# Optimization experiments

Hardware: AMD Instinct MI355X
Metric: run time of the kernel (lower is better)

Reference implementation:

```python
import jax, jax.numpy as jnp
import numpy as np

EPS = 1e-6
NH, HD, D, FF = 4, 128, 512, 2048
SCALE = HD ** -0.5


def rms(x, w):
    return x * jax.lax.rsqrt(jnp.mean(x * x, axis=-1, keepdims=True) + EPS) * w


def adaln(x, emb, w, b, nw):
    e = jax.nn.silu(emb) @ w.T + b  # [B, 6D]
    sm, cm, gm, sp, cp, gp = jnp.split(e, 6, axis=-1)
    y = rms(x, nw) * (1.0 + cm[:, None]) + sm[:, None]
    return y, gm, sp, cp, gp


def apply_rope(x, rope):
    # x: [B,H,N,HD], rope: [N,1,HD] (even slots cos-source, odd slots sin-source)
    f = rope[:, 0]  # [N, HD]
    cos = jnp.repeat(f[:, 0::2], 2, axis=-1)[None, None]  # [1,1,N,HD]
    sin = jnp.repeat(f[:, 1::2], 2, axis=-1)[None, None]
    xr = x.reshape(*x.shape[:-1], -1, 2)
    rot = jnp.stack([-xr[..., 1], xr[..., 0]], axis=-1).reshape(x.shape)
    return x * cos + rot * sin


def sdpa(q, k, v, scale):
    s = jnp.einsum('bhqd,bhkd->bhqk', q, k) * scale
    p = jax.nn.softmax(s, axis=-1)
    return jnp.einsum('bhqk,bhkd->bhqd', p, v)


def mlp(x, w1, b1, w2, b2):
    h = jax.nn.gelu(x @ w1.T + b1, approximate=True)
    return h @ w2.T + b2


def setup_inputs() -> dict:
    key = jax.random.key(0)
    ks = jax.random.split(key, 32)
    B, L, Hh, Ww = 2, 512, 64, 32
    N = Hh * Ww
    s = 1.0 / np.sqrt(D)
    sf = 1.0 / np.sqrt(FF)
    rn = lambda k, sh, sc=1.0: jax.random.normal(k, sh, jnp.float32) * sc
    # RoPE buffer: per-pair angles, even slots cos, odd slots sin
    pos = jnp.arange(N, dtype=jnp.float32)
    inv = 1.0 / (10000.0 ** (jnp.arange(0, HD, 2, dtype=jnp.float32) / HD))
    ang = pos[:, None] * inv[None, :]  # [N, HD//2]
    rope = jnp.zeros((N, 1, HD), jnp.float32)
    rope = rope.at[:, 0, 0::2].set(jnp.cos(ang)).at[:, 0, 1::2].set(jnp.sin(ang))
    return {
        'txt': rn(ks[0], (B, L, D)),
        'img': rn(ks[1], (B, N, D)),
        'vec': rn(ks[2], (B, D)),
        'rope': rope,
        'sol_temperature': jax.random.uniform(ks[3], (B, NH), jnp.float32) + 0.5,
        'sol_spatial': rn(ks[4], (B, 8, 8)),
        'img_adaln_w': rn(ks[5], (6 * D, D), s), 'img_adaln_b': rn(ks[6], (6 * D,), 0.02),
        'img_adaln_norm_w': jnp.ones((D,), jnp.float32),
        'txt_adaln_w': rn(ks[7], (6 * D, D), s), 'txt_adaln_b': rn(ks[8], (6 * D,), 0.02),
        'txt_adaln_norm_w': jnp.ones((D,), jnp.float32),
        'txt_qkv_w': rn(ks[9], (3 * NH * HD, D), s),
        'img_qkv_w': rn(ks[10], (3 * NH * HD, D), s),
        'txt_out_w': rn(ks[11], (D, NH * HD), s),
        'img_out_w': rn(ks[12], (D, NH * HD), s),
        'sol_mod_w': rn(ks[13], (NH,), 0.1), 'sol_mod_b': rn(ks[14], (NH,), 0.1),
        'img_norm2_w': jnp.ones((D,), jnp.float32),
        'txt_norm2_w': jnp.ones((D,), jnp.float32),
        'img_fc1_w': rn(ks[15], (FF, D), s), 'img_fc1_b': rn(ks[16], (FF,), 0.02),
        'img_fc2_w': rn(ks[17], (D, FF), sf), 'img_fc2_b': rn(ks[18], (D,), 0.02),
        'txt_fc1_w': rn(ks[19], (FF, D), s), 'txt_fc1_b': rn(ks[20], (FF,), 0.02),
        'txt_fc2_w': rn(ks[21], (D, FF), sf), 'txt_fc2_b': rn(ks[22], (D,), 0.02),
        'H': Hh, 'W': Ww,
    }


def reference(txt, img, vec, rope, sol_temperature, sol_spatial,
              img_adaln_w, img_adaln_b, img_adaln_norm_w,
              txt_adaln_w, txt_adaln_b, txt_adaln_norm_w,
              txt_qkv_w, img_qkv_w, txt_out_w, img_out_w,
              sol_mod_w, sol_mod_b, img_norm2_w, txt_norm2_w,
              img_fc1_w, img_fc1_b, img_fc2_w, img_fc2_b,
              txt_fc1_w, txt_fc1_b, txt_fc2_w, txt_fc2_b, H, W):
    B, L, _ = txt.shape
    N = img.shape[1]
    img_n, img_g, img_sh, img_sc, img_gm = adaln(img, vec, img_adaln_w, img_adaln_b, img_adaln_norm_w)
    txt_n, txt_g, txt_sh, txt_sc, txt_gm = adaln(txt, vec, txt_adaln_w, txt_adaln_b, txt_adaln_norm_w)
    # joint attention
    tqkv = (txt_n @ txt_qkv_w.T).reshape(B, L, 3, NH, HD)
    iqkv = (img_n @ img_qkv_w.T).reshape(B, N, 3, NH, HD)
    tq, tk, tv = [jnp.transpose(tqkv[:, :, i], (0, 2, 1, 3)) for i in range(3)]
    iq, ik, iv = [jnp.transpose(iqkv[:, :, i], (0, 2, 1, 3)) for i in range(3)]
    iq = apply_rope(iq, rope)
    ik = apply_rope(ik, rope)
    # spatial prior modulation (1x1 conv over bilinear-upsampled prior)
    sol_up = jax.image.resize(sol_spatial[:, None], (B, 1, H, W), method='bilinear')
    mod = sol_up * sol_mod_w[None, :, None, None] + sol_mod_b[None, :, None, None]  # [B,NH,H,W]
    mod = jnp.exp(jnp.clip(mod.reshape(B, NH, H * W), -2.0, 2.0))
    iq = iq * mod[..., None]
    ik = ik * mod[..., None]
    k = jnp.concatenate([tk, ik], axis=2)  # [B,NH,L+N,HD]
    v = jnp.concatenate([tv, iv], axis=2)
    txt_att = sdpa(tq, k, v, SCALE)
    txt_att = jnp.transpose(txt_att, (0, 2, 1, 3)).reshape(B, L, NH * HD) @ txt_out_w.T
    # temperature-rescaled image attention
    temp = jnp.maximum(jnp.mean(sol_temperature, axis=1, keepdims=True), 0.1)  # [B,1]
    eff = (SCALE / temp)[:, :, None, None]  # [B,1,1,1]
    img_att = sdpa(iq * jnp.sqrt(eff), k * jnp.sqrt(eff), v, 1.0)
    img_att = jnp.transpose(img_att, (0, 2, 1, 3)).reshape(B, N, NH * HD) @ img_out_w.T
    txt = txt + txt_g[:, None] * txt_att
    img = img + img_g[:, None] * img_att
    txt_in = rms(txt, txt_norm2_w) * (1.0 + txt_sc[:, None]) + txt_sh[:, None]
    img_in = rms(img, img_norm2_w) * (1.0 + img_sc[:, None]) + img_sh[:, None]
    txt = txt + txt_gm[:, None] * mlp(txt_in, txt_fc1_w, txt_fc1_b, txt_fc2_w, txt_fc2_b)
    img = img + img_gm[:, None] * mlp(img_in, img_fc1_w, img_fc1_b, img_fc2_w, img_fc2_b)
    return (txt, img)
```

## Files before the change

### kernel.cpp

```cpp
#include <hip/hip_runtime.h>
#include <math.h>

typedef unsigned short ushort_t;

constexpr int B_  = 2;
constexpr int L_  = 512;
constexpr int N_  = 2048;
constexpr int T_  = 2560;
constexpr int D_  = 512;
constexpr int NH_ = 4;
constexpr int HD_ = 128;
constexpr int FF_ = 2048;
constexpr int SIXD = 3072;
constexpr int MROWS = B_ * T_;
#define SCALE_ 0.08838834764831843f

constexpr size_t QSZ    = (size_t)B_ * NH_ * T_ * HD_;
constexpr size_t O_ETXT = 0;
constexpr size_t O_EIMG = O_ETXT + (size_t)B_ * SIXD;
constexpr size_t O_MOD  = O_EIMG + (size_t)B_ * SIXD;
constexpr size_t O_EFF  = O_MOD + (size_t)B_ * NH_ * N_;
constexpr size_t O_XN   = O_EFF + 16;
constexpr size_t O_Q    = O_XN + QSZ;
constexpr size_t O_K    = O_Q + QSZ;
constexpr size_t O_V    = O_K + QSZ;
constexpr size_t O_ATTN = O_V + QSZ;
constexpr size_t O_X2   = O_ATTN + QSZ;
constexpr size_t O_XIN2 = O_X2 + QSZ;
constexpr size_t O_H    = O_Q;
constexpr size_t O_ML   = O_X2 + QSZ / 2;

constexpr size_t WQ_STREAM = (size_t)SIXD / 2 * D_;
constexpr size_t WQ_TOTAL  = 2 * WQ_STREAM;
constexpr size_t WM_PROJ   = 0;
constexpr size_t WM_PROJ_S = (size_t)D_ * D_;
constexpr size_t WM_FC1    = WM_PROJ + 2 * WM_PROJ_S;
constexpr size_t WM_FC1_S  = (size_t)FF_ * D_;
constexpr size_t WM_FC2    = WM_FC1 + 2 * WM_FC1_S;
constexpr size_t WM_FC2_S  = (size_t)D_ * FF_;

typedef short bf16x8 __attribute__((ext_vector_type(8)));
typedef float f32x4 __attribute__((ext_vector_type(4)));

__device__ __forceinline__ ushort_t f2bf_rne(float x) {
  unsigned u = __float_as_uint(x);
  u += 0x7fff + ((u >> 16) & 1);
  return (ushort_t)(u >> 16);
}

__device__ __forceinline__ void gload_lds16(const ushort_t* g, ushort_t* l) {
  __builtin_amdgcn_global_load_lds(
      (const __attribute__((address_space(1))) void*)g,
      (__attribute__((address_space(3))) void*)l, 16, 0, 0);
}

__global__ __launch_bounds__(256) void k_stage0(
    const float* __restrict__ vec,
    const float* __restrict__ wt, const float* __restrict__ bt,
    const float* __restrict__ wi, const float* __restrict__ bi,
    const float* __restrict__ sspat, const float* __restrict__ mw,
    const float* __restrict__ mb, const float* __restrict__ stemp,
    const float* __restrict__ qkvwt, const float* __restrict__ qkvwi,
    float* __restrict__ ws) {
  int blk = blockIdx.x;
  if (blk < 48) {
    int s = blk / 24;
    int rem = blk % 24;
    int b = rem / 12;
    int o = (rem % 12) * 256 + threadIdx.x;
    __shared__ float sv[D_];
    for (int i = threadIdx.x; i < D_; i += 256) {
      float x = vec[b * D_ + i];
      sv[i] = x / (1.0f + __expf(-x));
    }
    __syncthreads();
    const float* w = (s == 0) ? wt : wi;
    const float* bb = (s == 0) ? bt : bi;
    const float4* wrow = (const float4*)(w + (size_t)o * D_);
    float acc = 0.f;
    for (int d4 = 0; d4 < D_ / 4; ++d4) {
      float4 wv = wrow[d4];
      int d = d4 * 4;
      acc += wv.x * sv[d] + wv.y * sv[d + 1] + wv.z * sv[d + 2] + wv.w * sv[d + 3];
    }
    acc += bb[o];
    float* e = ws + ((s == 0) ? O_ETXT : O_EIMG);
    e[b * SIXD + o] = acc;
  } else if (blk < 112) {
    int idx = (blk - 48) * 256 + threadIdx.x;
    if (idx < B_) {
      float s = 0.f;
      for (int h = 0; h < NH_; ++h) s += stemp[idx * NH_ + h];
      float t = fmaxf(s * 0.25f, 0.1f);
      ws[O_EFF + idx] = SCALE_ / t;
    }
    int b = idx / (NH_ * N_);
    int h = (idx / N_) % NH_;
    int n = idx % N_;
    int y = n >> 5;
    int x = n & 31;
    float fy = (y + 0.5f) * 0.125f - 0.5f;
    float fx = (x + 0.5f) * 0.25f  - 0.5f;
    float y0f = floorf(fy), x0f = floorf(fx);
    float wy = fy - y0f, wx = fx - x0f;
    int y0 = (int)y0f, x0 = (int)x0f;
    int iy0 = y0 < 0 ? 0 : y0, iy1 = (y0 + 1) > 7 ? 7 : (y0 + 1);
    int ix0 = x0 < 0 ? 0 : x0, ix1 = (x0 + 1) > 7 ? 7 : (x0 + 1);
    const float* S = sspat + b * 64;
    float v00 = S[iy0*8+ix0], v01 = S[iy0*8+ix1];
    float v10 = S[iy1*8+ix0], v11 = S[iy1*8+ix1];
    float up = (1.f-wy)*((1.f-wx)*v00 + wx*v01) + wy*((1.f-wx)*v10 + wx*v11);
    float m = up * mw[h] + mb[h];
    m = fminf(fmaxf(m, -2.f), 2.f);
    ws[O_MOD + idx] = __expf(m);
  } else {
    int g = (blk - 112) * 256 + threadIdx.x;
    int s = g >= (int)(WQ_STREAM / 4);
    const float4* src = (const float4*)(s ? qkvwi : qkvwt);
    float4 v = src[g - s * (int)(WQ_STREAM / 4)];
    ushort4 hh, ll;
    hh.x = f2bf_rne(v.x); hh.y = f2bf_rne(v.y); hh.z = f2bf_rne(v.z); hh.w = f2bf_rne(v.w);
    ll.x = f2bf_rne(v.x - __uint_as_float((unsigned)hh.x << 16));
    ll.y = f2bf_rne(v.y - __uint_as_float((unsigned)hh.y << 16));
    ll.z = f2bf_rne(v.z - __uint_as_float((unsigned)hh.z << 16));
    ll.w = f2bf_rne(v.w - __uint_as_float((unsigned)hh.w << 16));
    ushort_t* Wqh = (ushort_t*)(ws + O_ATTN);
    ushort_t* Wql = Wqh + WQ_TOTAL;
    *(ushort4*)&Wqh[(size_t)g * 4] = hh;
    *(ushort4*)&Wql[(size_t)g * 4] = ll;
  }
}

template<bool FROM_INPUT>
__global__ __launch_bounds__(256) void k_rmsmod(const float* __restrict__ txt, const float* __restrict__ img,
                                                const float* __restrict__ src_ws,
                                                const float* __restrict__ nw_txt, const float* __restrict__ nw_img,
                                                int sh_off, int sc_off,
                                                const float* __restrict__ e_ws,
                                                ushort_t* __restrict__ oh, ushort_t* __restrict__ ol) {
  int row = blockIdx.x;
  int b = row / T_;
  int t = row % T_;
  bool is_txt = t < L_;
  int i0 = threadIdx.x * 2;
  float x0, x1;
  if (FROM_INPUT) {
    const float* src = is_txt ? (txt + ((size_t)b * L_ + t) * D_)
                              : (img + ((size_t)b * N_ + (t - L_)) * D_);
    x0 = src[i0]; x1 = src[i0 + 1];
  } else {
    const float* src = src_ws + (size_t)row * D_;
    x0 = src[i0]; x1 = src[i0 + 1];
  }
  float ss = x0 * x0 + x1 * x1;
  for (int off = 32; off; off >>= 1) ss += __shfl_down(ss, off, 64);
  __shared__ float red[4];
  if ((threadIdx.x & 63) == 0) red[threadIdx.x >> 6] = ss;
  __syncthreads();
  float tot = red[0] + red[1] + red[2] + red[3];
  float r = rsqrtf(tot * (1.0f / D_) + 1e-6f);
  const float* e = e_ws + (is_txt ? O_ETXT : O_EIMG) + (size_t)b * SIXD;
  const float* nw = is_txt ? nw_txt : nw_img;
  float y0 = x0 * r * nw[i0]     * (1.f + e[sc_off + i0])     + e[sh_off + i0];
  float y1 = x1 * r * nw[i0 + 1] * (1.f + e[sc_off + i0 + 1]) + e[sh_off + i0 + 1];
  ushort_t h0 = f2bf_rne(y0), h1 = f2bf_rne(y1);
  ushort_t l0 = f2bf_rne(y0 - __uint_as_float((unsigned)h0 << 16));
  ushort_t l1 = f2bf_rne(y1 - __uint_as_float((unsigned)h1 << 16));
  *(unsigned*)&oh[(size_t)row * D_ + i0] = (unsigned)h0 | ((unsigned)h1 << 16);
  *(unsigned*)&ol[(size_t)row * D_ + i0] = (unsigned)l0 | ((unsigned)l1 << 16);
}

template<int NTILE, int NTERMS, int KDIM, int NPR, int EPI>
__global__ __launch_bounds__(256) void k_gemm(
    const ushort_t* __restrict__ Aph, const ushort_t* __restrict__ Apl,
    const ushort_t* __restrict__ Wth, const ushort_t* __restrict__ Wtl,
    const ushort_t* __restrict__ Wih, const ushort_t* __restrict__ Wil,
    const float* __restrict__ biast, const float* __restrict__ biasi,
    const float* __restrict__ ws_ro, float* __restrict__ wsw,
    const float* __restrict__ txt, const float* __restrict__ img,
    ushort_t* __restrict__ Hph, ushort_t* __restrict__ Hpl, float* __restrict__ outf) {
  int mt = blockIdx.x / NPR, nt = blockIdx.x % NPR;
  int row0 = mt * 128;
  int col0 = nt * NTILE;
  int b = row0 / T_;
  int t0 = row0 % T_;
  bool is_txt = t0 < L_;
  const ushort_t* Wh = is_txt ? Wth : Wih;
  const ushort_t* Wl = (NTERMS == 3) ? (is_txt ? Wtl : Wil) : nullptr;

  __shared__ __align__(16) ushort_t ash[128 * 32];
  __shared__ __align__(16) ushort_t asl[128 * 32];
  __shared__ __align__(16) ushort_t bsh[NTILE * 32];
  __shared__ __align__(16) ushort_t bsl[(NTERMS == 3) ? NTILE * 32 : 8];

  int tid = threadIdx.x;
  int w = tid >> 6, lane = tid & 63, quad = lane >> 4, lc = lane & 15;
  int rh = w >> 1, ch = w & 1;
  constexpr int NFR = NTILE / 32;

  int Rloc  = lane >> 2;
  int lslot = (lane & 3) ^ ((lane >> 3) & 3);
  int ssw = (quad ^ ((lc >> 1) & 3)) * 8;

  f32x4 acc[4][NFR];
  #pragma unroll
  for (int m = 0; m < 4; ++m)
    #pragma unroll
    for (int n = 0; n < NFR; ++n) acc[m][n] = f32x4{0.f, 0.f, 0.f, 0.f};

  for (int kt = 0; kt < KDIM / 32; ++kt) {
    int scol = kt * 32 + lslot * 8;
    #pragma unroll
    for (int cc = 0; cc < 2; ++cc) {
      int c = w * 2 + cc;
      size_t goff = (size_t)(row0 + c * 16 + Rloc) * KDIM + scol;
      gload_lds16(Aph + goff, &ash[c * 512]);
      gload_lds16(Apl + goff, &asl[c * 512]);
    }
    #pragma unroll
    for (int cc = 0; cc < NTILE / 64; ++cc) {
      int c = w + cc * 4;
      size_t goff = (size_t)(col0 + c * 16 + Rloc) * KDIM + scol;
      gload_lds16(Wh + goff, &bsh[c * 512]);
      if (NTERMS == 3) gload_lds16(Wl + goff, &bsl[c * 512]);
    }
    __syncthreads();

    bf16x8 afh[4], afl[4];
    #pragma unroll
    for (int m = 0; m < 4; ++m) {
      int ar = rh * 64 + m * 16 + lc;
      afh[m] = *(const bf16x8*)&ash[ar * 32 + ssw];
      afl[m] = *(const bf16x8*)&asl[ar * 32 + ssw];
    }
    #pragma unroll
    for (int n = 0; n < NFR; ++n) {
      int br = ch * (NTILE / 2) + n * 16 + lc;
      bf16x8 bh = *(const bf16x8*)&bsh[br * 32 + ssw];
      if (NTERMS == 3) {
        bf16x8 bl = *(const bf16x8*)&bsl[br * 32 + ssw];
        #pragma unroll
        for (int m = 0; m < 4; ++m) {
          acc[m][n] = __builtin_amdgcn_mfma_f32_16x16x32_bf16(afl[m], bh, acc[m][n], 0, 0, 0);
          acc[m][n] = __builtin_amdgcn_mfma_f32_16x16x32_bf16(afh[m], bl, acc[m][n], 0, 0, 0);
          acc[m][n] = __builtin_amdgcn_mfma_f32_16x16x32_bf16(afh[m], bh, acc[m][n], 0, 0, 0);
        }
      } else {
        #pragma unroll
        for (int m = 0; m < 4; ++m) {
          acc[m][n] = __builtin_amdgcn_mfma_f32_16x16x32_bf16(afl[m], bh, acc[m][n], 0, 0, 0);
          acc[m][n] = __builtin_amdgcn_mfma_f32_16x16x32_bf16(afh[m], bh, acc[m][n], 0, 0, 0);
        }
      }
    }
    __syncthreads();
  }

  const float* e = ws_ro + (is_txt ? O_ETXT : O_EIMG) + (size_t)b * SIXD;
  const float* bias = is_txt ? biast : biasi;
  #pragma unroll
  for (int m = 0; m < 4; ++m) {
    #pragma unroll
    for (int n = 0; n < NFR; ++n) {
      #pragma unroll
      for (int r = 0; r < 4; ++r) {
        int rg = row0 + rh * 64 + m * 16 + quad * 4 + r;
        int cg = col0 + ch * (NTILE / 2) + n * 16 + lc;
        float val = acc[m][n][r];
        int tt = rg % T_;
        if (EPI == 0) {
          int which = cg >> 9, h = (cg >> 7) & 3, dd = cg & 127;
          float* dst = wsw + (which == 0 ? O_Q : which == 1 ? O_K : O_V)
                     + (((size_t)b * NH_ + h) * T_ + tt) * HD_ + dd;
          *dst = val;
        } else if (EPI == 1) {
          float g = e[1024 + cg];
          float res = is_txt ? txt[((size_t)b * L_ + tt) * D_ + cg]
                             : img[((size_t)b * N_ + (tt - L_)) * D_ + cg];
          wsw[O_X2 + (size_t)rg * D_ + cg] = res + g * val;
        } else if (EPI == 2) {
          float x = val + bias[cg];
          float z = 0.7978845608028654f * (x + 0.044715f * x * x * x);
          z = fminf(fmaxf(z, -40.f), 40.f);
          float u = __expf(-2.f * z);
          float th = (1.f - u) / (1.f + u);
          float hv = 0.5f * x * (1.f + th);
          ushort_t hh = f2bf_rne(hv);
          Hph[(size_t)rg * FF_ + cg] = hh;
          Hpl[(size_t)rg * FF_ + cg] = f2bf_rne(hv - __uint_as_float((unsigned)hh << 16));
        } else {
          float g = e[2560 + cg];
          float v2 = ws_ro[O_X2 + (size_t)rg * D_ + cg] + g * (val + bias[cg]);
          size_t oi = is_txt ? ((size_t)b * L_ + tt) * D_ + cg
                             : (size_t)B_ * L_ * D_ + ((size_t)b * N_ + (tt - L_)) * D_ + cg;
          outf[oi] = v2;
        }
      }
    }
  }
}

__global__ __launch_bounds__(256) void k_stage1(
    float* __restrict__ ws, const float* __restrict__ rope,
    const float* __restrict__ pw_t, const float* __restrict__ pw_i,
    const float* __restrict__ f1_t, const float* __restrict__ f1_i,
    const float* __restrict__ f2_t, const float* __restrict__ f2_i) {
  int blk = blockIdx.x;
  if (blk < 5120) {
    int idx = blk * 256 + threadIdx.x;
    int i = idx & 63;
    int p = idx >> 6;
    int t = p % T_;
    int bh = p / T_;
    size_t base = (size_t)p * HD_ + 2 * i;
    float* Q = ws + O_Q;
    float* K = ws + O_K;
    float k0 = K[base], k1 = K[base + 1];
    if (t >= L_) {
      int n = t - L_;
      float c = rope[(size_t)n * HD_ + 2 * i];
      float s = rope[(size_t)n * HD_ + 2 * i + 1];
      float m = ws[O_MOD + (size_t)bh * N_ + n];
      float q0 = Q[base], q1 = Q[base + 1];
      Q[base]     = (q0 * c - q1 * s) * m;
      Q[base + 1] = (q1 * c + q0 * s) * m;
      float nk0 = (k0 * c - k1 * s) * m;
      float nk1 = (k1 * c + k0 * s) * m;
      k0 = nk0; k1 = nk1;
    }
    ushort_t h0 = f2bf_rne(k0), h1 = f2bf_rne(k1);
    ushort_t l0 = f2bf_rne(k0 - __uint_as_float((unsigned)h0 << 16));
    ushort_t l1 = f2bf_rne(k1 - __uint_as_float((unsigned)h1 << 16));
    ushort_t* KH = (ushort_t*)(ws + O_XIN2);
    ushort_t* KL = KH + QSZ;
    *(unsigned*)&KH[(size_t)p * HD_ + 2 * i] = (unsigned)h0 | ((unsigned)h1 << 16);
    *(unsigned*)&KL[(size_t)p * HD_ + 2 * i] = (unsigned)l0 | ((unsigned)l1 << 16);
  } else if (blk < 5440) {
    int vblk = blk - 5120;
    int bh = vblk & 7;
    int tt = vblk >> 3;
    int t0 = tt * 64;
    __shared__ ushort_t vls[128 * 72];
    int tid = threadIdx.x;
    {
      int tr = tid & 63, dc = tid >> 6;
      const float4* src = (const float4*)(ws + O_V + ((size_t)bh * T_ + t0 + tr) * HD_ + dc * 32);
      #pragma unroll
      for (int f = 0; f < 8; ++f) {
        float4 v = src[f];
        int d = dc * 32 + f * 4;
        vls[(d + 0) * 72 + tr] = f2bf_rne(v.x);
        vls[(d + 1) * 72 + tr] = f2bf_rne(v.y);
        vls[(d + 2) * 72 + tr] = f2bf_rne(v.z);
        vls[(d + 3) * 72 + tr] = f2bf_rne(v.w);
      }
    }
    __syncthreads();
    {
      int d = tid >> 1, th = (tid & 1) * 32;
      unsigned* Vt32 = (unsigned*)(ws + O_X2);
      size_t obase = (((size_t)bh * HD_ + d) * T_ + t0 + th) >> 1;
      #pragma unroll
      for (int k = 0; k < 16; ++k) {
        unsigned lo = vls[d * 72 + th + 2 * k];
        unsigned hi = vls[d * 72 + th + 2 * k + 1];
        Vt32[obase + k] = lo | (hi << 16);
      }
    }
  } else {
    int g = (blk - 5440) * 256 + threadIdx.x;
    const float* src; int local;
    if (g < 65536)        { src = pw_t; local = g; }
    else if (g < 131072)  { src = pw_i; local = g - 65536; }
    else if (g < 393216)  { src = f1_t; local = g - 131072; }
    else if (g < 655360)  { src = f1_i; local = g - 393216; }
    else if (g < 917504)  { src = f2_t; local = g - 655360; }
    else                  { src = f2_i; local = g - 917504; }
    float4 v = ((const float4*)src)[local];
    ushort4 hh;
    hh.x = f2bf_rne(v.x); hh.y = f2bf_rne(v.y); hh.z = f2bf_rne(v.z); hh.w = f2bf_rne(v.w);
    ushort_t* Wm = (ushort_t*)(ws + O_XN);
    *(ushort4*)&Wm[(size_t)g * 4] = hh;
  }
}

__global__ __launch_bounds__(256) void k_attn7(const float* __restrict__ ws_ro, float* __restrict__ wsw) {
  int bh = blockIdx.x & 7;
  int rest = blockIdx.x >> 3;
  int qg = rest % 40;
  int ks = rest / 40;
  int kt0 = (ks == 0) ? 0 : (ks == 1) ? 14 : 27;
  int kt1 = (ks == 0) ? 14 : (ks == 1) ? 27 : 40;
  int b = bh >> 2;
  int tid = threadIdx.x;
  int w = tid >> 6, lane = tid & 63, quad = lane >> 4, lc = lane & 15;
  int q0 = (qg * 4 + w) * 16;
  float scale = (q0 < L_) ? SCALE_ : ws_ro[O_EFF + b];

  const ushort_t* Khs = (const ushort_t*)(ws_ro + O_XIN2);
  const ushort_t* Kls = Khs + QSZ;
  const ushort_t* Vts = (const ushort_t*)(ws_ro + O_X2) + (size_t)bh * HD_ * T_;

  __shared__ __align__(16) ushort_t ksh[64 * 136];
  __shared__ __align__(16) ushort_t ksl[64 * 136];
  __shared__ __align__(16) ushort_t ps[4 * 16 * 72];
  ushort_t* pw = &ps[w * 1152];

  bf16x8 qh[4], ql[4];
  {
    const float* qrowp = ws_ro + O_Q + ((size_t)bh * T_ + q0 + lc) * HD_ + quad * 8;
    #pragma unroll
    for (int k2 = 0; k2 < 4; ++k2) {
      float4 a = *(const float4*)(qrowp + k2 * 32);
      float4 c = *(const float4*)(qrowp + k2 * 32 + 4);
      float v[8] = {a.x, a.y, a.z, a.w, c.x, c.y, c.z, c.w};
      #pragma unroll
      for (int e = 0; e < 8; ++e) {
        float x = v[e] * scale;
        ushort_t hh = f2bf_rne(x);
        float hf = __uint_as_float((unsigned)hh << 16);
        qh[k2][e] = (short)hh;
        ql[k2][e] = (short)f2bf_rne(x - hf);
      }
    }
  }

  f32x4 o[8];
  #pragma unroll
  for (int i = 0; i < 8; ++i) o[i] = f32x4{0.f, 0.f, 0.f, 0.f};
  float m_r[4] = {-1e30f, -1e30f, -1e30f, -1e30f};
  float l_r[4] = {0.f, 0.f, 0.f, 0.f};

  for (int kt = kt0; kt < kt1; ++kt) {
    {
      int row = tid >> 2, cs = tid & 3;
      size_t gbase = ((size_t)bh * T_ + kt * 64 + row) * HD_;
      #pragma unroll
      for (int cc = 0; cc < 4; ++cc) {
        int c = cs + cc * 4;
        *(uint4*)&ksh[row * 136 + c * 8] = *(const uint4*)&Khs[gbase + c * 8];
        *(uint4*)&ksl[row * 136 + c * 8] = *(const uint4*)&Kls[gbase + c * 8];
      }
    }
    __syncthreads();

    f32x4 s[4];
    #pragma unroll
    for (int nt = 0; nt < 4; ++nt) s[nt] = f32x4{0.f, 0.f, 0.f, 0.f};
    #pragma unroll
    for (int k2 = 0; k2 < 4; ++k2) {
      int ko = k2 * 32 + quad * 8;
      #pragma unroll
      for (int nt = 0; nt < 4; ++nt) {
        bf16x8 kh = *(const bf16x8*)&ksh[(nt * 16 + lc) * 136 + ko];
        bf16x8 kl = *(const bf16x8*)&ksl[(nt * 16 + lc) * 136 + ko];
        s[nt] = __builtin_amdgcn_mfma_f32_16x16x32_bf16(ql[k2], kh, s[nt], 0, 0, 0);
        s[nt] = __builtin_amdgcn_mfma_f32_16x16x32_bf16(qh[k2], kl, s[nt], 0, 0, 0);
        s[nt] = __builtin_amdgcn_mfma_f32_16x16x32_bf16(qh[k2], kh, s[nt], 0, 0, 0);
      }
    }

    const ushort_t* Vb = Vts + kt * 64;
    bf16x8 vb0[8];
    #pragma unroll
    for (int dt = 0; dt < 8; ++dt)
      vb0[dt] = *(const bf16x8*)&Vb[(size_t)(dt * 16 + lc) * T_ + quad * 8];

    float alpha[4];
    #pragma unroll
    for (int r = 0; r < 4; ++r) {
      float rm = fmaxf(fmaxf(s[0][r], s[1][r]), fmaxf(s[2][r], s[3][r]));
      rm = fmaxf(rm, __shfl_xor(rm, 1, 64));
      rm = fmaxf(rm, __shfl_xor(rm, 2, 64));
      rm = fmaxf(rm, __shfl_xor(rm, 4, 64));
      rm = fmaxf(rm, __shfl_xor(rm, 8, 64));
      float mn = fmaxf(m_r[r], rm);
      alpha[r] = __expf(m_r[r] - mn);
      m_r[r] = mn;
      float p0 = __expf(s[0][r] - mn);
      float p1 = __expf(s[1][r] - mn);
      float p2 = __expf(s[2][r] - mn);
      float p3 = __expf(s[3][r] - mn);
      float rs = (p0 + p1) + (p2 + p3);
      rs += __shfl_xor(rs, 1, 64);
      rs += __shfl_xor(rs, 2, 64);
      rs += __shfl_xor(rs, 4, 64);
      rs += __shfl_xor(rs, 8, 64);
      l_r[r] = l_r[r] * alpha[r] + rs;
      int prow = quad * 4 + r;
      pw[prow * 72 + lc]      = f2bf_rne(p0);
      pw[prow * 72 + lc + 16] = f2bf_rne(p1);
      pw[prow * 72 + lc + 32] = f2bf_rne(p2);
      pw[prow * 72 + lc + 48] = f2bf_rne(p3);
    }
    #pragma unroll
    for (int dt = 0; dt < 8; ++dt) {
      #pragma unroll
      for (int r = 0; r < 4; ++r) o[dt][r] *= alpha[r];
    }

    bf16x8 vb1[8];
    #pragma unroll
    for (int dt = 0; dt < 8; ++dt)
      vb1[dt] = *(const bf16x8*)&Vb[(size_t)(dt * 16 + lc) * T_ + 32 + quad * 8];

    bf16x8 pa0 = *(const bf16x8*)&pw[lc * 72 + quad * 8];
    bf16x8 pa1 = *(const bf16x8*)&pw[lc * 72 + 32 + quad * 8];
    #pragma unroll
    for (int dt = 0; dt < 8; ++dt)
      o[dt] = __builtin_amdgcn_mfma_f32_16x16x32_bf16(pa0, vb0[dt], o[dt], 0, 0, 0);
    #pragma unroll
    for (int dt = 0; dt < 8; ++dt)
      o[dt] = __builtin_amdgcn_mfma_f32_16x16x32_bf16(pa1, vb1[dt], o[dt], 0, 0, 0);
    __syncthreads();
  }

  float* OP = wsw + ((ks == 0) ? O_K : (ks == 1) ? O_V : O_ATTN);
  float* ML = wsw + O_ML;
  int trow0 = q0 + quad * 4;
  #pragma unroll
  for (int r = 0; r < 4; ++r) {
    size_t base = ((size_t)bh * T_ + (trow0 + r)) * HD_ + lc;
    #pragma unroll
    for (int dt = 0; dt < 8; ++dt) OP[base + dt * 16] = o[dt][r];
    if (lc == 0) {
      size_t mi = (((size_t)ks * 8 + bh) * T_ + (trow0 + r)) * 2;
      ML[mi]     = m_r[r];
      ML[mi + 1] = l_r[r];
    }
  }
}

__global__ __launch_bounds__(256) void k_comb(const float* __restrict__ ws_ro, float* __restrict__ wsw) {
  int bh = blockIdx.x & 7;
  int qg = blockIdx.x >> 3;
  int b = bh >> 2, h = bh & 3;
  int q0 = qg * 64;
  int tid = threadIdx.x;
  __shared__ float wls[64][4];
  if (tid < 64) {
    const float* ML = ws_ro + O_ML;
    size_t r0 = ((size_t)0 * 8 + bh) * T_ + q0 + tid;
    size_t r1 = ((size_t)1 * 8 + bh) * T_ + q0 + tid;
    size_t r2 = ((size_t)2 * 8 + bh) * T_ + q0 + tid;
    float m0 = ML[r0 * 2], l0 = ML[r0 * 2 + 1];
    float m1 = ML[r1 * 2], l1 = ML[r1 * 2 + 1];
    float m2 = ML[r2 * 2], l2 = ML[r2 * 2 + 1];
    float mm = fmaxf(fmaxf(m0, m1), m2);
    float w0 = __expf(m0 - mm), w1 = __expf(m1 - mm), w2 = __expf(m2 - mm);
    float inv = 1.0f / (w0 * l0 + w1 * l1 + w2 * l2);
    wls[tid][0] = w0 * inv; wls[tid][1] = w1 * inv; wls[tid][2] = w2 * inv; wls[tid][3] = 0.f;
  }
  __syncthreads();
  const float* P0 = ws_ro + O_K;
  const float* P1 = ws_ro + O_V;
  const float* P2 = ws_ro + O_ATTN;
  ushort_t* ATh = (ushort_t*)(wsw + O_Q);
  ushort_t* ATl = ATh + QSZ;
  #pragma unroll
  for (int it = 0; it < 8; ++it) {
    int idx = it * 256 + tid;
    int row = idx >> 5;
    int d4 = (idx & 31) * 4;
    size_t pb = ((size_t)bh * T_ + q0 + row) * HD_ + d4;
    float4 a = *(const float4*)&P0[pb];
    float4 c = *(const float4*)&P1[pb];
    float4 d = *(const float4*)&P2[pb];
    float w0 = wls[row][0], w1 = wls[row][1], w2 = wls[row][2];
    float v[4] = {a.x * w0 + c.x * w1 + d.x * w2,
                  a.y * w0 + c.y * w1 + d.y * w2,
                  a.z * w0 + c.z * w1 + d.z * w2,
                  a.w * w0 + c.w * w1 + d.w * w2};
    ushort4 hh, ll;
    ushort_t* hp = (ushort_t*)&hh; ushort_t* lp = (ushort_t*)&ll;
    #pragma unroll
    for (int j = 0; j < 4; ++j) {
      ushort_t hv = f2bf_rne(v[j]);
      hp[j] = hv;
      lp[j] = f2bf_rne(v[j] - __uint_as_float((unsigned)hv << 16));
    }
    size_t ob = ((size_t)b * T_ + q0 + row) * D_ + h * HD_ + d4;
    *(ushort4*)&ATh[ob] = hh;
    *(ushort4*)&ATl[ob] = ll;
  }
}

extern "C" void kernel_launch(void* const* d_in, const int* in_sizes, int n_in,
                              void* d_out, int out_size, void* d_ws, size_t ws_size,
                              hipStream_t stream) {
  (void)in_sizes; (void)n_in; (void)out_size; (void)ws_size;
  const float* txt    = (const float*)d_in[0];
  const float* img    = (const float*)d_in[1];
  const float* vec    = (const float*)d_in[2];
  const float* rope   = (const float*)d_in[3];
  const float* stemp  = (const float*)d_in[4];
  const float* sspat  = (const float*)d_in[5];
  const float* i_aw   = (const float*)d_in[6];
  const float* i_ab   = (const float*)d_in[7];
  const float* i_anw  = (const float*)d_in[8];
  const float* t_aw   = (const float*)d_in[9];
  const float* t_ab   = (const float*)d_in[10];
  const float* t_anw  = (const float*)d_in[11];
  const float* t_qkvw = (const float*)d_in[12];
  const float* i_qkvw = (const float*)d_in[13];
  const float* t_outw = (const float*)d_in[14];
  const float* i_outw = (const float*)d_in[15];
  const float* modw   = (const float*)d_in[16];
  const float* modb   = (const float*)d_in[17];
  const float* i_n2w  = (const float*)d_in[18];
  const float* t_n2w  = (const float*)d_in[19];
  const float* i_f1w  = (const float*)d_in[20];
  const float* i_f1b  = (const float*)d_in[21];
  const float* i_f2w  = (const float*)d_in[22];
  const float* i_f2b  = (const float*)d_in[23];
  const float* t_f1w  = (const float*)d_in[24];
  const float* t_f1b  = (const float*)d_in[25];
  const float* t_f2w  = (const float*)d_in[26];
  const float* t_f2b  = (const float*)d_in[27];
  float* ws = (float*)d_ws;
  float* out = (float*)d_out;
  ushort_t* XNh  = (ushort_t*)(ws + O_XN);   ushort_t* XNl  = XNh + QSZ;
  ushort_t* XI2h = (ushort_t*)(ws + O_XIN2); ushort_t* XI2l = XI2h + QSZ;
  ushort_t* Hh   = (ushort_t*)(ws + O_H);    ushort_t* Hl   = Hh + 4 * QSZ;
  ushort_t* ATh  = (ushort_t*)(ws + O_Q);    ushort_t* ATl  = ATh + QSZ;
  ushort_t* Wqh = (ushort_t*)(ws + O_ATTN);  ushort_t* Wql = Wqh + WQ_TOTAL;
  ushort_t* Wm  = (ushort_t*)(ws + O_XN);

  hipLaunchKernelGGL(k_stage0, dim3(48 + 64 + 1536), dim3(256), 0, stream,
                     vec, t_aw, t_ab, i_aw, i_ab, sspat, modw, modb, stemp,
                     t_qkvw, i_qkvw, ws);
  hipLaunchKernelGGL((k_rmsmod<true>), dim3(MROWS), dim3(256), 0, stream,
                     txt, img, (const float*)nullptr, t_anw, i_anw, 0, 512, ws, XNh, XNl);
  hipLaunchKernelGGL((k_gemm<128, 3, 512, 12, 0>), dim3(40 * 12), dim3(256), 0, stream,
                     XNh, XNl, Wqh, Wql, Wqh + WQ_STREAM, Wql + WQ_STREAM,
                     nullptr, nullptr, ws, ws, txt, img,
                     (ushort_t*)nullptr, (ushort_t*)nullptr, nullptr);
  hipLaunchKernelGGL(k_stage1, dim3(5120 + 320 + 4608), dim3(256), 0, stream,
                     ws, rope, t_outw, i_outw, t_f1w, i_f1w, t_f2w, i_f2w);
  hipLaunchKernelGGL(k_attn7, dim3(960), dim3(256), 0, stream, ws, ws);
  hipLaunchKernelGGL(k_comb, dim3(320), dim3(256), 0, stream, ws, ws);
  hipLaunchKernelGGL((k_gemm<64, 2, 512, 8, 1>), dim3(40 * 8), dim3(256), 0, stream,
                     ATh, ATl, Wm + WM_PROJ, nullptr, Wm + WM_PROJ + WM_PROJ_S, nullptr,
                     nullptr, nullptr, ws, ws, txt, img,
                     (ushort_t*)nullptr, (ushort_t*)nullptr, nullptr);
  hipLaunchKernelGGL((k_rmsmod<false>), dim3(MROWS), dim3(256), 0, stream,
                     (const float*)nullptr, (const float*)nullptr, ws + O_X2, t_n2w, i_n2w,
                     1536, 2048, ws, XI2h, XI2l);
  hipLaunchKernelGGL((k_gemm<128, 2, 512, 16, 2>), dim3(40 * 16), dim3(256), 0, stream,
                     XI2h, XI2l, Wm + WM_FC1, nullptr, Wm + WM_FC1 + WM_FC1_S, nullptr,
                     t_f1b, i_f1b, ws, ws, txt, img, Hh, Hl, nullptr);
  hipLaunchKernelGGL((k_gemm<64, 2, 2048, 8, 3>), dim3(40 * 8), dim3(256), 0, stream,
                     Hh, Hl, Wm + WM_FC2, nullptr, Wm + WM_FC2 + WM_FC2_S, nullptr,
                     t_f2b, i_f2b, ws, ws, txt, img,
                     (ushort_t*)nullptr, (ushort_t*)nullptr, out);
}
```

Before: 490.3 us.

## Prefetch next K tile into LDS via direct global-to-LDS loads with XOR swizzle

The attention kernel now loads K hi/lo tiles straight from global memory into LDS using direct-to-LDS 16-byte loads. The padded row stride is replaced by an XOR-swizzled unpadded layout to avoid bank conflicts. The load for the next key tile is issued right after the QK^T MFMAs, so it overlaps with the softmax and PV work of the current tile and hides global latency. This relies on correct wait/barrier placement before the next iteration reads the buffer.

```diff
diff --git a/kernel.cpp b/kernel.cpp
--- a/kernel.cpp
+++ b/kernel.cpp
@@ -384,7 +384,7 @@
   }
 }
 
-__global__ __launch_bounds__(256) void k_attn7(const float* __restrict__ ws_ro, float* __restrict__ wsw) {
+__global__ __launch_bounds__(256) void k_attn10(const float* __restrict__ ws_ro, float* __restrict__ wsw) {
   int bh = blockIdx.x & 7;
   int rest = blockIdx.x >> 3;
   int qg = rest % 40;
@@ -401,10 +401,13 @@
   const ushort_t* Kls = Khs + QSZ;
   const ushort_t* Vts = (const ushort_t*)(ws_ro + O_X2) + (size_t)bh * HD_ * T_;
 
-  __shared__ __align__(16) ushort_t ksh[64 * 136];
-  __shared__ __align__(16) ushort_t ksl[64 * 136];
+  __shared__ __align__(16) ushort_t ksh[64 * 128];
+  __shared__ __align__(16) ushort_t ksl[64 * 128];
   __shared__ __align__(16) ushort_t ps[4 * 16 * 72];
   ushort_t* pw = &ps[w * 1152];
+
+  int rloc = lane >> 4;
+  int sst  = lane & 15;
 
   bf16x8 qh[4], ql[4];
   {
@@ -431,32 +434,47 @@
   float m_r[4] = {-1e30f, -1e30f, -1e30f, -1e30f};
   float l_r[4] = {0.f, 0.f, 0.f, 0.f};
 
+  {
+    size_t gRow = (size_t)bh * T_ + kt0 * 64;
+    #pragma unroll
+    for (int j = 0; j < 4; ++j) {
+      int r0 = w * 16 + j * 4;
+      int lslot = sst ^ (j * 4 + rloc);
+      size_t goff = (gRow + r0 + rloc) * HD_ + (size_t)lslot * 8;
+      gload_lds16(Khs + goff, &ksh[r0 * 128]);
+      gload_lds16(Kls + goff, &ksl[r0 * 128]);
+    }
+  }
+  __syncthreads();
+
   for (int kt = kt0; kt < kt1; ++kt) {
-    {
-      int row = tid >> 2, cs = tid & 3;
-      size_t gbase = ((size_t)bh * T_ + kt * 64 + row) * HD_;
-      #pragma unroll
-      for (int cc = 0; cc < 4; ++cc) {
-        int c = cs + cc * 4;
-        *(uint4*)&ksh[row * 136 + c * 8] = *(const uint4*)&Khs[gbase + c * 8];
-        *(uint4*)&ksl[row * 136 + c * 8] = *(const uint4*)&Kls[gbase + c * 8];
-      }
-    }
-    __syncthreads();
-
     f32x4 s[4];
     #pragma unroll
     for (int nt = 0; nt < 4; ++nt) s[nt] = f32x4{0.f, 0.f, 0.f, 0.f};
     #pragma unroll
     for (int k2 = 0; k2 < 4; ++k2) {
-      int ko = k2 * 32 + quad * 8;
       #pragma unroll
       for (int nt = 0; nt < 4; ++nt) {
-        bf16x8 kh = *(const bf16x8*)&ksh[(nt * 16 + lc) * 136 + ko];
-        bf16x8 kl = *(const bf16x8*)&ksl[(nt * 16 + lc) * 136 + ko];
+        int row = nt * 16 + lc;
+        int so = ((k2 * 4 + quad) ^ lc) * 8;
+        bf16x8 kh = *(const bf16x8*)&ksh[row * 128 + so];
+        bf16x8 kl = *(const bf16x8*)&ksl[row * 128 + so];
         s[nt] = __builtin_amdgcn_mfma_f32_16x16x32_bf16(ql[k2], kh, s[nt], 0, 0, 0);
         s[nt] = __builtin_amdgcn_mfma_f32_16x16x32_bf16(qh[k2], kl, s[nt], 0, 0, 0);
         s[nt] = __builtin_amdgcn_mfma_f32_16x16x32_bf16(qh[k2], kh, s[nt], 0, 0, 0);
+      }
+    }
+    __syncthreads();
+
+    if (kt + 1 < kt1) {
+      size_t gRow = (size_t)bh * T_ + (kt + 1) * 64;
+      #pragma unroll
+      for (int j = 0; j < 4; ++j) {
+        int r0 = w * 16 + j * 4;
+        int lslot = sst ^ (j * 4 + rloc);
+        size_t goff = (gRow + r0 + rloc) * HD_ + (size_t)lslot * 8;
+        gload_lds16(Khs + goff, &ksh[r0 * 128]);
+        gload_lds16(Kls + goff, &ksl[r0 * 128]);
       }
     }
 
@@ -637,7 +655,7 @@
                      (ushort_t*)nullptr, (ushort_t*)nullptr, nullptr);
   hipLaunchKernelGGL(k_stage1, dim3(5120 + 320 + 4608), dim3(256), 0, stream,
                      ws, rope, t_outw, i_outw, t_f1w, i_f1w, t_f2w, i_f2w);
-  hipLaunchKernelGGL(k_attn7, dim3(960), dim3(256), 0, stream, ws, ws);
+  hipLaunchKernelGGL(k_attn10, dim3(960), dim3(256), 0, stream, ws, ws);
   hipLaunchKernelGGL(k_comb, dim3(320), dim3(256), 0, stream, ws, ws);
   hipLaunchKernelGGL((k_gemm<64, 2, 512, 8, 1>), dim3(40 * 8), dim3(256), 0, stream,
                      ATh, ATl, Wm + WM_PROJ, nullptr, Wm + WM_PROJ + WM_PROJ_S, nullptr,
```

New measurement: 483.1 us. About the same (-1.5%).
